# Optimization experiments

Measured on AMD Instinct MI355X. Metric: run time of the kernel, lower is better.

The kernel has to match this reference:

```python
import jax, jax.numpy as jnp
import numpy as np

MAX_LEN = 2048

def setup_inputs() -> dict:
    key = jax.random.key(0)
    k1, k2, k3 = jax.random.split(key, 3)
    B, S, E, V, C = 32, 2048, 512, 50257, 2
    x = jax.random.randint(k1, (B, S), 0, V, dtype=jnp.int64)
    emb_table = jax.random.normal(k2, (V, E), dtype=jnp.float32) * 0.02
    fc_w = jax.random.normal(k3, (C, E), dtype=jnp.float32) * 0.02
    fc_b = jnp.zeros((C,), dtype=jnp.float32)
    return {"x": x, "emb_table": emb_table, "fc_w": fc_w, "fc_b": fc_b}

def reference(x, emb_table, fc_w, fc_b):
    x = x[:, :MAX_LEN]                               # [B,S]
    x_emb = emb_table[x]                             # [B,S,E]
    scores = jnp.einsum('bse,bte->bst', x_emb, x_emb)  # [B,S,S] unscaled
    attn = jax.nn.softmax(scores, axis=-1)
    attended = jnp.einsum('bst,bte->bse', attn, x_emb)  # [B,S,E]
    pooled = attended.max(axis=1)                    # pool='max' -> [B,E]
    return pooled @ fc_w.T + fc_b                    # [B,C]
```

## Files before the change

kernel.cpp:

```cpp
#include <hip/hip_runtime.h>
#include <float.h>


typedef __attribute__((ext_vector_type(8))) short short8;
typedef __attribute__((ext_vector_type(4))) float f32x4;
typedef __attribute__((ext_vector_type(16))) float f32x16;
typedef __attribute__((ext_vector_type(4))) short s16x4;

__device__ __forceinline__ short f2bf(float f) {
  unsigned u = __float_as_uint(f);
  unsigned r = (u + 0x7fffu + ((u >> 16) & 1u)) >> 16;
  return (short)r;
}
__device__ __forceinline__ float bf2f(short s) {
  return __uint_as_float(((unsigned)(unsigned short)s) << 16);
}
__device__ __forceinline__ unsigned f2e4m3(float f) {
  unsigned u = __float_as_uint(f);
  unsigned s = (u >> 31) << 7;
  int exp = (int)((u >> 23) & 0xff) - 127;
  unsigned m = (u & 0x7fffff) | 0x800000;
  if (exp < -10) return s;
  int shift = 20, e4 = 0;
  if (exp >= -6) e4 = exp + 7;
  else shift += (-6 - exp);
  unsigned keep = m >> shift;
  unsigned rem = m & ((1u << shift) - 1u);
  unsigned half = 1u << (shift - 1);
  keep += (rem > half || (rem == half && (keep & 1)));
  unsigned out;
  if (e4 > 0) {
    if (keep >= 16) { keep >>= 1; e4++; }
    out = ((unsigned)e4 << 3) | (keep & 7);
  } else {
    out = (keep >= 8) ? ((1u << 3) | (keep & 7)) : keep;
  }
  return s | out;
}
__device__ __forceinline__ unsigned ordf(float f) {
  unsigned u = __float_as_uint(f);
  return (u & 0x80000000u) ? ~u : (u | 0x80000000u);
}
__device__ __forceinline__ float unordf(unsigned e) {
  unsigned u = (e & 0x80000000u) ? (e ^ 0x80000000u) : ~e;
  return __uint_as_float(u);
}
__device__ __forceinline__ void gload16(const void* g, void* s) {
  __builtin_amdgcn_global_load_lds((const __attribute__((address_space(1))) void*)g,
                                   (__attribute__((address_space(3))) void*)s,
                                   16, 0, 0);
}
__device__ __forceinline__ unsigned pkbf(float lo, float hi) {
  unsigned r;
  asm("v_cvt_pk_bf16_f32 %0, %1, %2" : "=v"(r) : "v"(lo), "v"(hi));
  return r;
}
#define PLSWAP(a, b) asm volatile("v_permlane32_swap_b32 %0, %1" : "+v"(a), "+v"(b))
__device__ __forceinline__ long long mklong(unsigned lo, unsigned hi) {
  return (long long)((((unsigned long long)hi) << 32) | lo);
}

extern "C" __global__ __launch_bounds__(256)
void prep4(const int* __restrict__ xp, const float* __restrict__ emb,
           unsigned char* __restrict__ Kf8, short* __restrict__ Vf) {
  __shared__ __align__(16) short ls[32 * 520];
  const int t = threadIdx.x, kt = blockIdx.x, b = blockIdx.y;
  {
    const int r = t >> 3, seg = t & 7;
    const float* src = emb + (long)xp[b * 2048 + kt * 32 + r] * 512 + seg * 64;
    short* ldst = ls + r * 520 + seg * 64;
#pragma unroll
    for (int i = 0; i < 8; ++i) {
      float4 fa = *(const float4*)(src + i * 8);
      float4 fb = *(const float4*)(src + i * 8 + 4);
      short8 v = { f2bf(fa.x), f2bf(fa.y), f2bf(fa.z), f2bf(fa.w),
                   f2bf(fb.x), f2bf(fb.y), f2bf(fb.z), f2bf(fb.w) };
      *(short8*)(ldst + i * 8) = v;
    }
  }
  __syncthreads();
  {
    const long chunkK = ((long)b * 64 + kt) * 16384;
#pragma unroll
    for (int i = 0; i < 4; ++i) {
      int j = t * 4 + i;
      int sp = j >> 6, lj = j & 63;
      int keyl = lj & 31, hi2 = lj >> 5;
      const short* row = ls + keyl * 520 + 8 * hi2;
      unsigned dw[4];
#pragma unroll
      for (int c2 = 0; c2 < 4; ++c2) {
        unsigned d = 0;
#pragma unroll
        for (int bb2 = 0; bb2 < 4; ++bb2) {
          int c = c2 * 4 + bb2;
          int e = 16 * (2 * sp + (c >> 3)) + (c & 7);
          d |= f2e4m3(bf2f(row[e])) << (8 * bb2);
        }
        dw[c2] = d;
      }
      *(uint4*)(Kf8 + chunkK + (long)j * 16) = (uint4){dw[0], dw[1], dw[2], dw[3]};
    }
  }
#pragma unroll
  for (int rr = 0; rr < 8; ++rr) {
    int j = rr * 256 + t;
    int eb = j >> 7, ks2 = (j >> 6) & 1, l = j & 63;
    int e32 = l & 31, hi = l >> 5;
    const short* colp = ls + (ks2 * 16 + hi * 8) * 520 + eb * 32 + e32;
    short8 v = { colp[0], colp[520], colp[1040], colp[1560],
                 colp[2080], colp[2600], colp[3120], colp[3640] };
    *(short8*)(Vf + ((long)(b * 2048 + eb * 128 + kt * 2 + ks2) * 64 + l) * 8) = v;
  }
}

extern "C" __global__ __launch_bounds__(512, 2)
void attn9(const unsigned char* __restrict__ Kf8, const short* __restrict__ Vf,
           unsigned* __restrict__ pooled) {
  __shared__ __align__(16) uint4 lq8[32 * 64];
  __shared__ __align__(16) uint4 lp4[2][32 * 64];
  __shared__ float lsm[512];

  const int t = threadIdx.x, l = t & 63, w = t >> 6;
  const int n = blockIdx.x;
  const int b = (n & 7) + ((n >> 8) << 3);
  const int qt = (n >> 3) & 31;
  const int q32 = l & 31, hi = l >> 5;

  {
    const unsigned char* src = Kf8 + ((long)b * 64 + 2 * qt) * 16384;
#pragma unroll
    for (int i = 0; i < 4; ++i) {
      int sw = i * 512 + w * 64;
      gload16(src + (long)(sw + l) * 16, lq8 + sw);
    }
  }

  const unsigned char* kc0 = Kf8 + ((long)b * 64 + w) * 16384 + (long)l * 16;
  const short* vpA = Vf + ((long)(b * 2048 + (2 * w) * 128) * 64 + l) * 8;
  const short* vpB = vpA + 128 * 512;

#define QK8(kv, sp)                                                           \
  {                                                                           \
    long long ak0 = mklong(kv.x, kv.y);                                       \
    long long ak1 = mklong(kv.z, kv.w);                                       \
    uint4 qa = lq8[(sp) * 64 + l];                                            \
    uint4 qb = lq8[(16 + (sp)) * 64 + l];                                     \
    S0 = __builtin_amdgcn_mfma_f32_32x32x16_fp8_fp8(ak0, mklong(qa.x, qa.y), S0, 0, 0, 0); \
    S1 = __builtin_amdgcn_mfma_f32_32x32x16_fp8_fp8(ak0, mklong(qb.x, qb.y), S1, 0, 0, 0); \
    S0 = __builtin_amdgcn_mfma_f32_32x32x16_fp8_fp8(ak1, mklong(qa.z, qa.w), S0, 0, 0, 0); \
    S1 = __builtin_amdgcn_mfma_f32_32x32x16_fp8_fp8(ak1, mklong(qb.z, qb.w), S1, 0, 0, 0); \
  }
#define PACK2(pb)                                                             \
  {                                                                           \
    unsigned a0 = pkbf(S0[0], S0[1]),   c0 = pkbf(S0[4], S0[5]);   PLSWAP(a0, c0); \
    unsigned a1 = pkbf(S0[2], S0[3]),   c1 = pkbf(S0[6], S0[7]);   PLSWAP(a1, c1); \
    unsigned a2 = pkbf(S0[8], S0[9]),   c2 = pkbf(S0[12], S0[13]); PLSWAP(a2, c2); \
    unsigned a3 = pkbf(S0[10], S0[11]), c3 = pkbf(S0[14], S0[15]); PLSWAP(a3, c3); \
    lp4[pb][(4 * w + 0) * 64 + l] = (uint4){a0, a1, c0, c1};                  \
    lp4[pb][(4 * w + 2) * 64 + l] = (uint4){a2, a3, c2, c3};                  \
    unsigned d0 = pkbf(S1[0], S1[1]),   e0 = pkbf(S1[4], S1[5]);   PLSWAP(d0, e0); \
    unsigned d1 = pkbf(S1[2], S1[3]),   e1 = pkbf(S1[6], S1[7]);   PLSWAP(d1, e1); \
    unsigned d2 = pkbf(S1[8], S1[9]),   e2 = pkbf(S1[12], S1[13]); PLSWAP(d2, e2); \
    unsigned d3 = pkbf(S1[10], S1[11]), e3 = pkbf(S1[14], S1[15]); PLSWAP(d3, e3); \
    lp4[pb][(4 * w + 1) * 64 + l] = (uint4){d0, d1, e0, e1};                  \
    lp4[pb][(4 * w + 3) * 64 + l] = (uint4){d2, d3, e2, e3};                  \
  }

  uint4 kA[8], kB[8];
#pragma unroll
  for (int i = 0; i < 8; ++i) kA[i] = *(const uint4*)(kc0 + i * 1024);
#pragma unroll
  for (int i = 0; i < 8; ++i) kB[i] = *(const uint4*)(kc0 + (8 + i) * 1024);

  short8 vb[8];
#pragma unroll
  for (int ks = 0; ks < 4; ++ks) {
    vb[2 * ks]     = *(const short8*)(vpA + (long)ks * 512);
    vb[2 * ks + 1] = *(const short8*)(vpB + (long)ks * 512);
  }

  __syncthreads();

  f32x16 acc[2][2];
#pragma unroll
  for (int eg = 0; eg < 2; ++eg)
#pragma unroll
    for (int qg = 0; qg < 2; ++qg)
#pragma unroll
      for (int r = 0; r < 16; ++r) acc[eg][qg][r] = 0.f;
  float lr0 = 0.f, lr1 = 0.f;
  f32x16 S0, S1;

#pragma unroll
  for (int r = 0; r < 16; ++r) { S0[r] = 0.f; S1[r] = 0.f; }
  {
    const unsigned char* kcn = kc0 + 131072;
    __builtin_amdgcn_s_setprio(1);
#pragma unroll
    for (int sp = 0; sp < 8; ++sp) {
      QK8(kA[sp], sp)
      kA[sp] = *(const uint4*)(kcn + sp * 1024);
    }
#pragma unroll
    for (int sp = 0; sp < 8; ++sp) {
      QK8(kB[sp], 8 + sp)
      kB[sp] = *(const uint4*)(kcn + (8 + sp) * 1024);
    }
    __builtin_amdgcn_s_setprio(0);
  }
  {
    float ps0 = 0.f, ps1 = 0.f;
#pragma unroll
    for (int r = 0; r < 16; ++r) {
      S0[r] = __expf(S0[r]); ps0 += S0[r];
      S1[r] = __expf(S1[r]); ps1 += S1[r];
    }
    lr0 += ps0; lr1 += ps1;
  }
  PACK2(0)
  asm volatile("s_waitcnt lgkmcnt(0)" ::: "memory");
  __builtin_amdgcn_s_barrier();

  for (int kt = 1; kt < 8; ++kt) {
    const short* lps = (const short*)lp4[(kt - 1) & 1];
    const unsigned char* kcn = kc0 + (long)((kt < 7) ? kt + 1 : 7) * 131072;
    const int base = (kt - 1) * 16;
#pragma unroll
    for (int r = 0; r < 16; ++r) { S0[r] = 0.f; S1[r] = 0.f; }
#pragma unroll
    for (int ks = 0; ks < 16; ++ks) {
      short8 pf0 = *(const short8*)(lps + ((ks * 2 + 0) * 64 + l) * 8);
      short8 pf1 = *(const short8*)(lps + ((ks * 2 + 1) * 64 + l) * 8);
      short8 v0 = vb[(ks & 3) * 2];
      short8 v1 = vb[(ks & 3) * 2 + 1];
      __builtin_amdgcn_s_setprio(1);
      acc[0][0] = __builtin_amdgcn_mfma_f32_32x32x16_bf16(v0, pf0, acc[0][0], 0, 0, 0);
      acc[0][1] = __builtin_amdgcn_mfma_f32_32x32x16_bf16(v0, pf1, acc[0][1], 0, 0, 0);
      acc[1][0] = __builtin_amdgcn_mfma_f32_32x32x16_bf16(v1, pf0, acc[1][0], 0, 0, 0);
      acc[1][1] = __builtin_amdgcn_mfma_f32_32x32x16_bf16(v1, pf1, acc[1][1], 0, 0, 0);
      if (ks < 8) {
        QK8(kA[ks], ks)
      } else {
        QK8(kB[ks - 8], ks)
      }
      __builtin_amdgcn_s_setprio(0);
      {
        int nk = base + ks + 4; if (nk > 127) nk = 127;
        vb[(ks & 3) * 2]     = *(const short8*)(vpA + (long)nk * 512);
        vb[(ks & 3) * 2 + 1] = *(const short8*)(vpB + (long)nk * 512);
      }
      if (ks < 8) kA[ks] = *(const uint4*)(kcn + ks * 1024);
      else        kB[ks - 8] = *(const uint4*)(kcn + ks * 1024);
    }
    {
      float ps0 = 0.f, ps1 = 0.f;
#pragma unroll
      for (int r = 0; r < 16; ++r) {
        S0[r] = __expf(S0[r]); ps0 += S0[r];
        S1[r] = __expf(S1[r]); ps1 += S1[r];
      }
      lr0 += ps0; lr1 += ps1;
    }
    PACK2(kt & 1)
    asm volatile("s_waitcnt lgkmcnt(0)" ::: "memory");
    __builtin_amdgcn_s_barrier();
  }

  {
    const short* lps = (const short*)lp4[1];
#pragma unroll
    for (int ks = 0; ks < 16; ++ks) {
      short8 pf0 = *(const short8*)(lps + ((ks * 2 + 0) * 64 + l) * 8);
      short8 pf1 = *(const short8*)(lps + ((ks * 2 + 1) * 64 + l) * 8);
      short8 v0 = vb[(ks & 3) * 2];
      short8 v1 = vb[(ks & 3) * 2 + 1];
      __builtin_amdgcn_s_setprio(1);
      acc[0][0] = __builtin_amdgcn_mfma_f32_32x32x16_bf16(v0, pf0, acc[0][0], 0, 0, 0);
      acc[0][1] = __builtin_amdgcn_mfma_f32_32x32x16_bf16(v0, pf1, acc[0][1], 0, 0, 0);
      acc[1][0] = __builtin_amdgcn_mfma_f32_32x32x16_bf16(v1, pf0, acc[1][0], 0, 0, 0);
      acc[1][1] = __builtin_amdgcn_mfma_f32_32x32x16_bf16(v1, pf1, acc[1][1], 0, 0, 0);
      __builtin_amdgcn_s_setprio(0);
      if (ks < 12) {
        int nk = 112 + ks + 4;
        vb[(ks & 3) * 2]     = *(const short8*)(vpA + (long)nk * 512);
        vb[(ks & 3) * 2 + 1] = *(const short8*)(vpB + (long)nk * 512);
      }
    }
  }

  lr0 += __shfl_xor(lr0, 32, 64);
  lr1 += __shfl_xor(lr1, 32, 64);
  __syncthreads();
  if (l < 32) {
    lsm[w * 32 + l] = lr0;
    lsm[256 + w * 32 + l] = lr1;
  }
  __syncthreads();
  float lt0 = lsm[q32], lt1 = lsm[256 + q32];
#pragma unroll
  for (int kg = 1; kg < 8; ++kg) {
    lt0 += lsm[kg * 32 + q32];
    lt1 += lsm[256 + kg * 32 + q32];
  }
  float ri0 = 1.0f / lt0, ri1 = 1.0f / lt1;
#pragma unroll
  for (int eg = 0; eg < 2; ++eg)
#pragma unroll
    for (int r = 0; r < 16; ++r) {
      float v = fmaxf(acc[eg][0][r] * ri0, acc[eg][1][r] * ri1);
      v = fmaxf(v, __shfl_xor(v, 1, 64));
      v = fmaxf(v, __shfl_xor(v, 2, 64));
      v = fmaxf(v, __shfl_xor(v, 4, 64));
      v = fmaxf(v, __shfl_xor(v, 8, 64));
      v = fmaxf(v, __shfl_xor(v, 16, 64));
      if (q32 == 0) {
        int e = (2 * w + eg) * 32 + (r & 3) + 8 * (r >> 2) + 4 * hi;
        atomicMax(&pooled[b * 512 + e], ordf(v));
      }
    }
}

#define LDKp 520
#define LDVp 40
#define LDPp 40
extern "C" __global__ __launch_bounds__(256, 2)
void attn_fb(const int* __restrict__ xp, const float* __restrict__ emb,
             unsigned* __restrict__ pooled) {
  __shared__ __align__(16) short lds_k[32 * LDKp];
  __shared__ __align__(16) short lds_vt[512 * LDVp];
  __shared__ __align__(16) short lds_p[64 * LDPp];
  const int t = threadIdx.x, l = t & 63, w = t >> 6;
  const int b = blockIdx.y;
  const int q0 = blockIdx.x * 64;
  const int L = l & 15, g = l >> 4;
  short8 qf[16];
  {
    int qq = q0 + w * 16 + L;
    const float* qrow = emb + (long)xp[b * 2048 + qq] * 512;
#pragma unroll
    for (int ec = 0; ec < 16; ++ec) {
      int e0 = ec * 32 + 8 * g;
      float4 fa = *(const float4*)(qrow + e0);
      float4 fb = *(const float4*)(qrow + e0 + 4);
      short8 v = { f2bf(fa.x), f2bf(fa.y), f2bf(fa.z), f2bf(fa.w),
                   f2bf(fb.x), f2bf(fb.y), f2bf(fb.z), f2bf(fb.w) };
      qf[ec] = v;
    }
  }
  f32x4 acc[32];
#pragma unroll
  for (int nt = 0; nt < 32; ++nt) acc[nt] = (f32x4){0.f, 0.f, 0.f, 0.f};
  float mrun[4] = {-FLT_MAX, -FLT_MAX, -FLT_MAX, -FLT_MAX};
  float lrun[4] = {0.f, 0.f, 0.f, 0.f};
  for (int kt = 0; kt < 64; ++kt) {
    __syncthreads();
    if (t < 128) {
#pragma unroll 4
      for (int i = 0; i < 32; ++i) {
        const float* krow = emb + (long)xp[b * 2048 + kt * 32 + i] * 512;
        float4 f = *(const float4*)(krow + 4 * t);
        s16x4 v = { f2bf(f.x), f2bf(f.y), f2bf(f.z), f2bf(f.w) };
        *(s16x4*)&lds_k[i * LDKp + 4 * t] = v;
      }
    } else {
      const int u = t - 128, lane_ = u & 63, half = u >> 6;
#pragma unroll 2
      for (int kq = 0; kq < 8; ++kq) {
        const int kbase = b * 2048 + kt * 32 + kq * 4;
        const float* r0 = emb + (long)xp[kbase + 0] * 512;
        const float* r1 = emb + (long)xp[kbase + 1] * 512;
        const float* r2 = emb + (long)xp[kbase + 2] * 512;
        const float* r3 = emb + (long)xp[kbase + 3] * 512;
#pragma unroll
        for (int seg = 0; seg < 4; ++seg) {
          int e = lane_ + 64 * (seg + 4 * half);
          s16x4 v = { f2bf(r0[e]), f2bf(r1[e]), f2bf(r2[e]), f2bf(r3[e]) };
          *(s16x4*)&lds_vt[e * LDVp + 4 * kq] = v;
        }
      }
    }
    __syncthreads();
    f32x4 s0 = {0.f, 0.f, 0.f, 0.f}, s1 = {0.f, 0.f, 0.f, 0.f};
#pragma unroll
    for (int ec = 0; ec < 16; ++ec) {
      short8 k0 = *(const short8*)&lds_k[L * LDKp + ec * 32 + 8 * g];
      short8 k1 = *(const short8*)&lds_k[(L + 16) * LDKp + ec * 32 + 8 * g];
      s0 = __builtin_amdgcn_mfma_f32_16x16x32_bf16(qf[ec], k0, s0, 0, 0, 0);
      s1 = __builtin_amdgcn_mfma_f32_16x16x32_bf16(qf[ec], k1, s1, 0, 0, 0);
    }
    float p0[4], p1[4], sc[4];
#pragma unroll
    for (int r = 0; r < 4; ++r) {
      float v = fmaxf(s0[r], s1[r]);
      v = fmaxf(v, __shfl_xor(v, 1, 64));
      v = fmaxf(v, __shfl_xor(v, 2, 64));
      v = fmaxf(v, __shfl_xor(v, 4, 64));
      v = fmaxf(v, __shfl_xor(v, 8, 64));
      float nm = fmaxf(mrun[r], v);
      sc[r] = expf(mrun[r] - nm);
      p0[r] = expf(s0[r] - nm);
      p1[r] = expf(s1[r] - nm);
      float rs = p0[r] + p1[r];
      rs += __shfl_xor(rs, 1, 64);
      rs += __shfl_xor(rs, 2, 64);
      rs += __shfl_xor(rs, 4, 64);
      rs += __shfl_xor(rs, 8, 64);
      lrun[r] = lrun[r] * sc[r] + rs;
      mrun[r] = nm;
    }
    if (__any(sc[0] < 1.f || sc[1] < 1.f || sc[2] < 1.f || sc[3] < 1.f)) {
      f32x4 sv = { sc[0], sc[1], sc[2], sc[3] };
#pragma unroll
      for (int nt = 0; nt < 32; ++nt) acc[nt] *= sv;
    }
#pragma unroll
    for (int r = 0; r < 4; ++r) {
      int row = w * 16 + g * 4 + r;
      lds_p[row * LDPp + L]      = f2bf(p0[r]);
      lds_p[row * LDPp + 16 + L] = f2bf(p1[r]);
    }
    asm volatile("s_waitcnt lgkmcnt(0)" ::: "memory");
    short8 pf = *(const short8*)&lds_p[(w * 16 + L) * LDPp + 8 * g];
#pragma unroll
    for (int nt = 0; nt < 32; ++nt) {
      short8 vf = *(const short8*)&lds_vt[(nt * 16 + L) * LDVp + 8 * g];
      acc[nt] = __builtin_amdgcn_mfma_f32_16x16x32_bf16(pf, vf, acc[nt], 0, 0, 0);
    }
  }
  __syncthreads();
  float inv[4];
#pragma unroll
  for (int r = 0; r < 4; ++r) inv[r] = 1.f / lrun[r];
  float* rbuf = (float*)lds_k;
#pragma unroll
  for (int nt = 0; nt < 32; ++nt) {
    f32x4 a = acc[nt];
    float c = fmaxf(fmaxf(a[0] * inv[0], a[1] * inv[1]),
                    fmaxf(a[2] * inv[2], a[3] * inv[3]));
    c = fmaxf(c, __shfl_xor(c, 16, 64));
    c = fmaxf(c, __shfl_xor(c, 32, 64));
    if (g == 0) rbuf[w * 512 + nt * 16 + L] = c;
  }
  __syncthreads();
  for (int j = t; j < 512; j += 256) {
    float v = fmaxf(fmaxf(rbuf[j], rbuf[512 + j]),
                    fmaxf(rbuf[1024 + j], rbuf[1536 + j]));
    atomicMax(&pooled[b * 512 + j], ordf(v));
  }
}

extern "C" __global__ void fc_small(const unsigned* __restrict__ pooled,
                                    const float* __restrict__ fw,
                                    const float* __restrict__ fb,
                                    float* __restrict__ out) {
  int t = threadIdx.x;
  if (t >= 64) return;
  int bb = t >> 1, c = t & 1;
  float s = fb[c];
  for (int e = 0; e < 512; ++e)
    s += unordf(pooled[bb * 512 + e]) * fw[c * 512 + e];
  out[t] = s;
}

extern "C" void kernel_launch(void* const* d_in, const int* in_sizes, int n_in,
                              void* d_out, int out_size, void* d_ws, size_t ws_size,
                              hipStream_t stream) {
  const int* xp    = (const int*)d_in[0];
  const float* emb = (const float*)d_in[1];
  const float* fw  = (const float*)d_in[2];
  const float* fb  = (const float*)d_in[3];
  unsigned* pooled = (unsigned*)d_ws;

  hipMemsetAsync(pooled, 0, 32 * 512 * sizeof(unsigned), stream);

  const size_t need = 65536ull + 33554432ull + 2ull * 33554432ull * sizeof(short);
  if (ws_size >= need) {
    unsigned char* Kf8 = (unsigned char*)d_ws + 65536;
    short* Vff = (short*)(Kf8 + 33554432);
    prep4<<<dim3(64, 32), 256, 0, stream>>>(xp, emb, Kf8, Vff);
    attn9<<<dim3(1024), 512, 0, stream>>>(Kf8, Vff, pooled);
  } else {
    attn_fb<<<dim3(32, 32), 256, 0, stream>>>(xp, emb, pooled);
  }
  fc_small<<<1, 64, 0, stream>>>(pooled, fw, fb, (float*)d_out);
}
```

Before: 312.1 us.

## Software-pipeline LDS loads, halve K register buffer, split QK accumulators

The attention kernel now prefetches the next P and Q fragments from LDS one step ahead of the MFMAs, so LDS latency is hidden behind matrix ops. The K register prefetch buffer drops from 16 to 8 entries, and the buffer is refilled with a half-tile lookahead. This frees VGPRs at the cost of less prefetch distance. The QK fp8 MFMAs are split into two independent accumulator chains per output (a/b), which are summed before the exp, to break the dependency between back-to-back MFMAs.

```diff
diff --git a/kernel.cpp b/kernel.cpp
--- a/kernel.cpp
+++ b/kernel.cpp
@@ -115,8 +115,8 @@
 }
 
 extern "C" __global__ __launch_bounds__(512, 2)
-void attn9(const unsigned char* __restrict__ Kf8, const short* __restrict__ Vf,
-           unsigned* __restrict__ pooled) {
+void attn10(const unsigned char* __restrict__ Kf8, const short* __restrict__ Vf,
+            unsigned* __restrict__ pooled) {
   __shared__ __align__(16) uint4 lq8[32 * 64];
   __shared__ __align__(16) uint4 lp4[2][32 * 64];
   __shared__ float lsm[512];
@@ -140,38 +140,34 @@
   const short* vpA = Vf + ((long)(b * 2048 + (2 * w) * 128) * 64 + l) * 8;
   const short* vpB = vpA + 128 * 512;
 
-#define QK8(kv, sp)                                                           \
+#define QK4(kv, cqa, cqb)                                                     \
   {                                                                           \
-    long long ak0 = mklong(kv.x, kv.y);                                       \
-    long long ak1 = mklong(kv.z, kv.w);                                       \
-    uint4 qa = lq8[(sp) * 64 + l];                                            \
-    uint4 qb = lq8[(16 + (sp)) * 64 + l];                                     \
-    S0 = __builtin_amdgcn_mfma_f32_32x32x16_fp8_fp8(ak0, mklong(qa.x, qa.y), S0, 0, 0, 0); \
-    S1 = __builtin_amdgcn_mfma_f32_32x32x16_fp8_fp8(ak0, mklong(qb.x, qb.y), S1, 0, 0, 0); \
-    S0 = __builtin_amdgcn_mfma_f32_32x32x16_fp8_fp8(ak1, mklong(qa.z, qa.w), S0, 0, 0, 0); \
-    S1 = __builtin_amdgcn_mfma_f32_32x32x16_fp8_fp8(ak1, mklong(qb.z, qb.w), S1, 0, 0, 0); \
+    long long ak0 = mklong((kv).x, (kv).y);                                   \
+    long long ak1 = mklong((kv).z, (kv).w);                                   \
+    S0a = __builtin_amdgcn_mfma_f32_32x32x16_fp8_fp8(ak0, mklong((cqa).x, (cqa).y), S0a, 0, 0, 0); \
+    S1a = __builtin_amdgcn_mfma_f32_32x32x16_fp8_fp8(ak0, mklong((cqb).x, (cqb).y), S1a, 0, 0, 0); \
+    S0b = __builtin_amdgcn_mfma_f32_32x32x16_fp8_fp8(ak1, mklong((cqa).z, (cqa).w), S0b, 0, 0, 0); \
+    S1b = __builtin_amdgcn_mfma_f32_32x32x16_fp8_fp8(ak1, mklong((cqb).z, (cqb).w), S1b, 0, 0, 0); \
   }
 #define PACK2(pb)                                                             \
   {                                                                           \
-    unsigned a0 = pkbf(S0[0], S0[1]),   c0 = pkbf(S0[4], S0[5]);   PLSWAP(a0, c0); \
-    unsigned a1 = pkbf(S0[2], S0[3]),   c1 = pkbf(S0[6], S0[7]);   PLSWAP(a1, c1); \
-    unsigned a2 = pkbf(S0[8], S0[9]),   c2 = pkbf(S0[12], S0[13]); PLSWAP(a2, c2); \
-    unsigned a3 = pkbf(S0[10], S0[11]), c3 = pkbf(S0[14], S0[15]); PLSWAP(a3, c3); \
+    unsigned a0 = pkbf(S0a[0], S0a[1]),   c0 = pkbf(S0a[4], S0a[5]);   PLSWAP(a0, c0); \
+    unsigned a1 = pkbf(S0a[2], S0a[3]),   c1 = pkbf(S0a[6], S0a[7]);   PLSWAP(a1, c1); \
+    unsigned a2 = pkbf(S0a[8], S0a[9]),   c2 = pkbf(S0a[12], S0a[13]); PLSWAP(a2, c2); \
+    unsigned a3 = pkbf(S0a[10], S0a[11]), c3 = pkbf(S0a[14], S0a[15]); PLSWAP(a3, c3); \
     lp4[pb][(4 * w + 0) * 64 + l] = (uint4){a0, a1, c0, c1};                  \
     lp4[pb][(4 * w + 2) * 64 + l] = (uint4){a2, a3, c2, c3};                  \
-    unsigned d0 = pkbf(S1[0], S1[1]),   e0 = pkbf(S1[4], S1[5]);   PLSWAP(d0, e0); \
-    unsigned d1 = pkbf(S1[2], S1[3]),   e1 = pkbf(S1[6], S1[7]);   PLSWAP(d1, e1); \
-    unsigned d2 = pkbf(S1[8], S1[9]),   e2 = pkbf(S1[12], S1[13]); PLSWAP(d2, e2); \
-    unsigned d3 = pkbf(S1[10], S1[11]), e3 = pkbf(S1[14], S1[15]); PLSWAP(d3, e3); \
+    unsigned d0 = pkbf(S1a[0], S1a[1]),   e0 = pkbf(S1a[4], S1a[5]);   PLSWAP(d0, e0); \
+    unsigned d1 = pkbf(S1a[2], S1a[3]),   e1 = pkbf(S1a[6], S1a[7]);   PLSWAP(d1, e1); \
+    unsigned d2 = pkbf(S1a[8], S1a[9]),   e2 = pkbf(S1a[12], S1a[13]); PLSWAP(d2, e2); \
+    unsigned d3 = pkbf(S1a[10], S1a[11]), e3 = pkbf(S1a[14], S1a[15]); PLSWAP(d3, e3); \
     lp4[pb][(4 * w + 1) * 64 + l] = (uint4){d0, d1, e0, e1};                  \
     lp4[pb][(4 * w + 3) * 64 + l] = (uint4){d2, d3, e2, e3};                  \
   }
 
-  uint4 kA[8], kB[8];
-#pragma unroll
-  for (int i = 0; i < 8; ++i) kA[i] = *(const uint4*)(kc0 + i * 1024);
-#pragma unroll
-  for (int i = 0; i < 8; ++i) kB[i] = *(const uint4*)(kc0 + (8 + i) * 1024);
+  uint4 kbuf[8];
+#pragma unroll
+  for (int i = 0; i < 8; ++i) kbuf[i] = *(const uint4*)(kc0 + i * 1024);
 
   short8 vb[8];
 #pragma unroll
@@ -190,22 +186,23 @@
 #pragma unroll
       for (int r = 0; r < 16; ++r) acc[eg][qg][r] = 0.f;
   float lr0 = 0.f, lr1 = 0.f;
-  f32x16 S0, S1;
-
-#pragma unroll
-  for (int r = 0; r < 16; ++r) { S0[r] = 0.f; S1[r] = 0.f; }
-  {
-    const unsigned char* kcn = kc0 + 131072;
+  f32x16 S0a, S0b, S1a, S1b;
+
+#pragma unroll
+  for (int r = 0; r < 16; ++r) { S0a[r] = 0.f; S0b[r] = 0.f; S1a[r] = 0.f; S1b[r] = 0.f; }
+  {
+    uint4 qa = lq8[0 * 64 + l], qb = lq8[16 * 64 + l];
     __builtin_amdgcn_s_setprio(1);
 #pragma unroll
-    for (int sp = 0; sp < 8; ++sp) {
-      QK8(kA[sp], sp)
-      kA[sp] = *(const uint4*)(kcn + sp * 1024);
-    }
-#pragma unroll
-    for (int sp = 0; sp < 8; ++sp) {
-      QK8(kB[sp], 8 + sp)
-      kB[sp] = *(const uint4*)(kcn + (8 + sp) * 1024);
+    for (int sp = 0; sp < 16; ++sp) {
+      uint4 cqa = qa, cqb = qb;
+      if (sp < 15) {
+        qa = lq8[(sp + 1) * 64 + l];
+        qb = lq8[(16 + sp + 1) * 64 + l];
+      }
+      QK4(kbuf[sp & 7], cqa, cqb)
+      kbuf[sp & 7] = (sp < 8) ? *(const uint4*)(kc0 + (sp + 8) * 1024)
+                              : *(const uint4*)(kc0 + 131072 + (sp - 8) * 1024);
     }
     __builtin_amdgcn_s_setprio(0);
   }
@@ -213,8 +210,8 @@
     float ps0 = 0.f, ps1 = 0.f;
 #pragma unroll
     for (int r = 0; r < 16; ++r) {
-      S0[r] = __expf(S0[r]); ps0 += S0[r];
-      S1[r] = __expf(S1[r]); ps1 += S1[r];
+      S0a[r] = __expf(S0a[r] + S0b[r]); ps0 += S0a[r];
+      S1a[r] = __expf(S1a[r] + S1b[r]); ps1 += S1a[r];
     }
     lr0 += ps0; lr1 += ps1;
   }
@@ -224,41 +221,47 @@
 
   for (int kt = 1; kt < 8; ++kt) {
     const short* lps = (const short*)lp4[(kt - 1) & 1];
-    const unsigned char* kcn = kc0 + (long)((kt < 7) ? kt + 1 : 7) * 131072;
+    const unsigned char* kcur = kc0 + (long)kt * 131072;
+    const unsigned char* kcn  = kc0 + (long)((kt < 7) ? kt + 1 : 7) * 131072;
     const int base = (kt - 1) * 16;
 #pragma unroll
-    for (int r = 0; r < 16; ++r) { S0[r] = 0.f; S1[r] = 0.f; }
+    for (int r = 0; r < 16; ++r) { S0a[r] = 0.f; S0b[r] = 0.f; S1a[r] = 0.f; S1b[r] = 0.f; }
+    short8 pf0 = *(const short8*)(lps + ((0 * 2 + 0) * 64 + l) * 8);
+    short8 pf1 = *(const short8*)(lps + ((0 * 2 + 1) * 64 + l) * 8);
+    uint4 qa = lq8[0 * 64 + l], qb = lq8[16 * 64 + l];
 #pragma unroll
     for (int ks = 0; ks < 16; ++ks) {
-      short8 pf0 = *(const short8*)(lps + ((ks * 2 + 0) * 64 + l) * 8);
-      short8 pf1 = *(const short8*)(lps + ((ks * 2 + 1) * 64 + l) * 8);
+      short8 cpf0 = pf0, cpf1 = pf1;
+      uint4 cqa = qa, cqb = qb;
+      if (ks < 15) {
+        pf0 = *(const short8*)(lps + (((ks + 1) * 2 + 0) * 64 + l) * 8);
+        pf1 = *(const short8*)(lps + (((ks + 1) * 2 + 1) * 64 + l) * 8);
+        qa = lq8[(ks + 1) * 64 + l];
+        qb = lq8[(16 + ks + 1) * 64 + l];
+      }
       short8 v0 = vb[(ks & 3) * 2];
       short8 v1 = vb[(ks & 3) * 2 + 1];
       __builtin_amdgcn_s_setprio(1);
-      acc[0][0] = __builtin_amdgcn_mfma_f32_32x32x16_bf16(v0, pf0, acc[0][0], 0, 0, 0);
-      acc[0][1] = __builtin_amdgcn_mfma_f32_32x32x16_bf16(v0, pf1, acc[0][1], 0, 0, 0);
-      acc[1][0] = __builtin_amdgcn_mfma_f32_32x32x16_bf16(v1, pf0, acc[1][0], 0, 0, 0);
-      acc[1][1] = __builtin_amdgcn_mfma_f32_32x32x16_bf16(v1, pf1, acc[1][1], 0, 0, 0);
-      if (ks < 8) {
-        QK8(kA[ks], ks)
-      } else {
-        QK8(kB[ks - 8], ks)
-      }
+      acc[0][0] = __builtin_amdgcn_mfma_f32_32x32x16_bf16(v0, cpf0, acc[0][0], 0, 0, 0);
+      acc[0][1] = __builtin_amdgcn_mfma_f32_32x32x16_bf16(v0, cpf1, acc[0][1], 0, 0, 0);
+      acc[1][0] = __builtin_amdgcn_mfma_f32_32x32x16_bf16(v1, cpf0, acc[1][0], 0, 0, 0);
+      acc[1][1] = __builtin_amdgcn_mfma_f32_32x32x16_bf16(v1, cpf1, acc[1][1], 0, 0, 0);
+      QK4(kbuf[ks & 7], cqa, cqb)
       __builtin_amdgcn_s_setprio(0);
       {
         int nk = base + ks + 4; if (nk > 127) nk = 127;
         vb[(ks & 3) * 2]     = *(const short8*)(vpA + (long)nk * 512);
         vb[(ks & 3) * 2 + 1] = *(const short8*)(vpB + (long)nk * 512);
       }
-      if (ks < 8) kA[ks] = *(const uint4*)(kcn + ks * 1024);
-      else        kB[ks - 8] = *(const uint4*)(kcn + ks * 1024);
+      kbuf[ks & 7] = (ks < 8) ? *(const uint4*)(kcur + (ks + 8) * 1024)
+                              : *(const uint4*)(kcn + (ks - 8) * 1024);
     }
     {
       float ps0 = 0.f, ps1 = 0.f;
 #pragma unroll
       for (int r = 0; r < 16; ++r) {
-        S0[r] = __expf(S0[r]); ps0 += S0[r];
-        S1[r] = __expf(S1[r]); ps1 += S1[r];
+        S0a[r] = __expf(S0a[r] + S0b[r]); ps0 += S0a[r];
+        S1a[r] = __expf(S1a[r] + S1b[r]); ps1 += S1a[r];
       }
       lr0 += ps0; lr1 += ps1;
     }
@@ -269,17 +272,22 @@
 
   {
     const short* lps = (const short*)lp4[1];
+    short8 pf0 = *(const short8*)(lps + ((0 * 2 + 0) * 64 + l) * 8);
+    short8 pf1 = *(const short8*)(lps + ((0 * 2 + 1) * 64 + l) * 8);
 #pragma unroll
     for (int ks = 0; ks < 16; ++ks) {
-      short8 pf0 = *(const short8*)(lps + ((ks * 2 + 0) * 64 + l) * 8);
-      short8 pf1 = *(const short8*)(lps + ((ks * 2 + 1) * 64 + l) * 8);
+      short8 cpf0 = pf0, cpf1 = pf1;
+      if (ks < 15) {
+        pf0 = *(const short8*)(lps + (((ks + 1) * 2 + 0) * 64 + l) * 8);
+        pf1 = *(const short8*)(lps + (((ks + 1) * 2 + 1) * 64 + l) * 8);
+      }
       short8 v0 = vb[(ks & 3) * 2];
       short8 v1 = vb[(ks & 3) * 2 + 1];
       __builtin_amdgcn_s_setprio(1);
-      acc[0][0] = __builtin_amdgcn_mfma_f32_32x32x16_bf16(v0, pf0, acc[0][0], 0, 0, 0);
-      acc[0][1] = __builtin_amdgcn_mfma_f32_32x32x16_bf16(v0, pf1, acc[0][1], 0, 0, 0);
-      acc[1][0] = __builtin_amdgcn_mfma_f32_32x32x16_bf16(v1, pf0, acc[1][0], 0, 0, 0);
-      acc[1][1] = __builtin_amdgcn_mfma_f32_32x32x16_bf16(v1, pf1, acc[1][1], 0, 0, 0);
+      acc[0][0] = __builtin_amdgcn_mfma_f32_32x32x16_bf16(v0, cpf0, acc[0][0], 0, 0, 0);
+      acc[0][1] = __builtin_amdgcn_mfma_f32_32x32x16_bf16(v0, cpf1, acc[0][1], 0, 0, 0);
+      acc[1][0] = __builtin_amdgcn_mfma_f32_32x32x16_bf16(v1, cpf0, acc[1][0], 0, 0, 0);
+      acc[1][1] = __builtin_amdgcn_mfma_f32_32x32x16_bf16(v1, cpf1, acc[1][1], 0, 0, 0);
       __builtin_amdgcn_s_setprio(0);
       if (ks < 12) {
         int nk = 112 + ks + 4;
@@ -479,7 +487,7 @@
     unsigned char* Kf8 = (unsigned char*)d_ws + 65536;
     short* Vff = (short*)(Kf8 + 33554432);
     prep4<<<dim3(64, 32), 256, 0, stream>>>(xp, emb, Kf8, Vff);
-    attn9<<<dim3(1024), 512, 0, stream>>>(Kf8, Vff, pooled);
+    attn10<<<dim3(1024), 512, 0, stream>>>(Kf8, Vff, pooled);
   } else {
     attn_fb<<<dim3(32, 32), 256, 0, stream>>>(xp, emb, pooled);
   }
```

After: 346.0 us. 10.9% more time.
